# Kernel optimization log

Hardware: AMD Instinct MI355X
Metric: run time of the kernel (lower is better)

The kernel has to match this reference:

```python
import jax, jax.numpy as jnp
import numpy as np

B, H, S, D = 2, 16, 2048, 128
BS = 128  # block_size
NB = S // BS  # num_blocks
SPARSITY_PROB = 0.5


def setup_inputs() -> dict:
    key = jax.random.key(0)
    kq, kk, kv, km = jax.random.split(key, 4)
    query = jax.random.normal(kq, (B, H, S, D), dtype=jnp.float32)
    k_ = jax.random.normal(kk, (B, H, S, D), dtype=jnp.float32)
    v_ = jax.random.normal(kv, (B, H, S, D), dtype=jnp.float32)
    # block pattern: rand < sparsity_prob, diagonal forced True (causal=False)
    block_mask = jax.random.uniform(km, (NB, NB)) < SPARSITY_PROB
    block_mask = block_mask | jnp.eye(NB, dtype=bool)
    return {"query": query, "key": k_, "value": v_,
            "block_mask": block_mask, "block_size": BS}


def reference(query, key, value, block_mask, block_size):
    b, h, s, d = query.shape
    nb = s // block_size
    scale = 1.0 / jnp.sqrt(jnp.float32(d))
    # reshape into blocks: (b, h, nb, bs, d)
    qb = query.reshape(b, h, nb, block_size, d)
    kb = key.reshape(b, h, nb, block_size, d)
    vb = value.reshape(b, h, nb, block_size, d)
    # per-(i,j)-block scores: (b, h, i, j, q, k)
    scores = jnp.einsum('bhiqd,bhjkd->bhijqk', qb, kb) * scale
    # IMPORTANT: softmax is taken independently within each block (axis=-1),
    # matching the original's per-block (non-merged) softmax.
    attn = jax.nn.softmax(scores, axis=-1)
    # zero out inactive blocks, then sum contributions over j
    attn = attn * block_mask[None, None, :, :, None, None].astype(attn.dtype)
    out = jnp.einsum('bhijqk,bhjkd->bhiqd', attn, vb)
    return out.reshape(b, h, s, d)
```

## Files before the change

### kernel.cpp

```cpp
#include <hip/hip_runtime.h>
#include <stdint.h>

#define CBDIM 256
#define WBDIM 256
#define DBDIM 512

#if __has_builtin(__builtin_amdgcn_permlane32_swap) && \
    __has_builtin(__builtin_amdgcn_permlane16_swap)
#define HAVE_PERMLANE_SWAP 1
#else
#define HAVE_PERMLANE_SWAP 0
#endif

typedef __attribute__((ext_vector_type(8))) short short8;
typedef __attribute__((ext_vector_type(4))) float f32x4;

__device__ __forceinline__ unsigned f2bf(float f) {
    union { float f; unsigned u; } a; a.f = f;
    unsigned r = a.u + 0x7fffu + ((a.u >> 16) & 1u);
    return (r >> 16) & 0xffffu;
}
__device__ __forceinline__ unsigned cvtpk_bf16(float a, float b) {
    unsigned r;
    asm("v_cvt_pk_bf16_f32 %0, %1, %2" : "=v"(r) : "v"(a), "v"(b));
    return r;
}
__device__ __forceinline__ float f4e(float4 v, int e) {
    return e == 0 ? v.x : e == 1 ? v.y : e == 2 ? v.z : v.w;
}
__device__ __forceinline__ unsigned u4e(uint4 v, int e) {
    return e == 0 ? v.x : e == 1 ? v.y : e == 2 ? v.z : v.w;
}
__device__ __forceinline__ uint2 shfl_u2(uint2 v, int src) {
    uint2 r;
    r.x = (unsigned)__shfl((int)v.x, src);
    r.y = (unsigned)__shfl((int)v.y, src);
    return r;
}
__device__ __forceinline__ float xor16_f(float x, int lane) {
#if HAVE_PERMLANE_SWAP
    unsigned u = __float_as_uint(x);
    auto r = __builtin_amdgcn_permlane16_swap(u, u, false, false);
    return __uint_as_float((lane & 16) ? r[0] : r[1]);
#else
    return __shfl_xor(x, 16);
#endif
}
__device__ __forceinline__ float xor32_f(float x, int lane) {
#if HAVE_PERMLANE_SWAP
    unsigned u = __float_as_uint(x);
    auto r = __builtin_amdgcn_permlane32_swap(u, u, false, false);
    return __uint_as_float((lane & 32) ? r[0] : r[1]);
#else
    return __shfl_xor(x, 32);
#endif
}
__device__ __forceinline__ bool detect_bf16(const void* p) {
    unsigned w = ((const unsigned*)p)[threadIdx.x & 63];
    unsigned lo = w & 0xffffu, ex = (lo >> 7) & 0xffu;
    bool pl = (lo == 0u) || (ex >= 0x68u && ex <= 0x86u);
    return __popcll(__ballot(pl)) >= 40;
}
__device__ __forceinline__ void gload_lds16(const void* g, void* l) {
    __builtin_amdgcn_global_load_lds(
        (const __attribute__((address_space(1))) void*)g,
        (__attribute__((address_space(3))) void*)l, 16, 0, 0);
}

__global__ __launch_bounds__(CBDIM)
void convert_fused(const void* __restrict__ Ksrc, const void* __restrict__ Vsrc,
                   uint4* __restrict__ Kw, uint4* __restrict__ Vt,
                   const unsigned char* __restrict__ Mb, int* __restrict__ order,
                   int nIdsK)
{
    const int tid = threadIdx.x;
    const int b = blockIdx.x;
    if (b < 512) {
        bool isBf = detect_bf16(Vsrc);
        if (b == 0 && tid < 64) {
            int tt = tid;
            unsigned mu = ((const unsigned*)Mb)[tt];
            bool maskByte = (__ballot((mu & 0xFFFFFF00u) != 0u) != 0ull);
            int cnt = 0;
            if (tt < 16)
                for (int j = 0; j < 16; ++j) {
                    bool a = maskByte ? (Mb[tt * 16 + j] != 0)
                                      : (((const int*)Mb)[tt * 16 + j] != 0);
                    cnt += a ? 1 : 0;
                }
            int rank = 0;
            for (int j = 0; j < 16; ++j) {
                int cj = __shfl(cnt, j);
                if (cj > cnt || (cj == cnt && j < tt)) ++rank;
            }
            if (tt < 16) order[rank] = tt;
        }
        const size_t kb = (size_t)b * 16384;
        char* base = (char*)(Vt + (size_t)b * 2048);
#pragma unroll
        for (int it = 0; it < 2; ++it) {
            int id = it * CBDIM + tid, pp = id & 31, dc = id >> 5;
            if (isBf) {
                const unsigned short* vb = (const unsigned short*)Vsrc + kb
                                           + (size_t)(4 * pp) * 128 + dc * 8;
                uint4 r0 = *(const uint4*)(vb);
                uint4 r1 = *(const uint4*)(vb + 128);
                uint4 r2 = *(const uint4*)(vb + 256);
                uint4 r3 = *(const uint4*)(vb + 384);
#pragma unroll
                for (int e = 0; e < 8; ++e) {
                    unsigned h0 = u4e(r0, e >> 1), h1 = u4e(r1, e >> 1);
                    unsigned h2 = u4e(r2, e >> 1), h3 = u4e(r3, e >> 1);
                    if (e & 1) { h0 >>= 16; h1 >>= 16; h2 >>= 16; h3 >>= 16; }
                    uint2 pk;
                    pk.x = (h0 & 0xffffu) | (h1 << 16);
                    pk.y = (h2 & 0xffffu) | (h3 << 16);
                    int d = dc * 8 + e;
                    *(uint2*)(base + d * 256 + (((pp >> 1) ^ (d & 7)) << 4)
                              + ((pp & 1) << 3)) = pk;
                }
            } else {
                const float* vb = (const float*)Vsrc + kb
                                  + (size_t)(4 * pp) * 128 + dc * 8;
                float4 ra[4], rb[4];
#pragma unroll
                for (int r = 0; r < 4; ++r) {
                    ra[r] = *(const float4*)(vb + (size_t)r * 128);
                    rb[r] = *(const float4*)(vb + (size_t)r * 128 + 4);
                }
#pragma unroll
                for (int e = 0; e < 8; ++e) {
                    float v0 = (e < 4) ? f4e(ra[0], e) : f4e(rb[0], e - 4);
                    float v1 = (e < 4) ? f4e(ra[1], e) : f4e(rb[1], e - 4);
                    float v2 = (e < 4) ? f4e(ra[2], e) : f4e(rb[2], e - 4);
                    float v3 = (e < 4) ? f4e(ra[3], e) : f4e(rb[3], e - 4);
                    uint2 pk;
                    pk.x = f2bf(v0) | (f2bf(v1) << 16);
                    pk.y = f2bf(v2) | (f2bf(v3) << 16);
                    int d = dc * 8 + e;
                    *(uint2*)(base + d * 256 + (((pp >> 1) ^ (d & 7)) << 4)
                              + ((pp & 1) << 3)) = pk;
                }
            }
        }
    } else {
        bool isBf = detect_bf16(Ksrc);
        int stride = ((int)gridDim.x - 512) * CBDIM;
        for (int id = (b - 512) * CBDIM + tid; id < nIdsK; id += stride) {
            int lid = id & 2047, tt = id >> 11;
            int r = lid >> 4, c = (lid & 15) ^ (r & 7);
            size_t eo = (size_t)tt * 16384 + (size_t)r * 128 + c * 8;
            uint4 w;
            if (isBf) {
                w = *(const uint4*)((const unsigned short*)Ksrc + eo);
            } else {
                const float* p = (const float*)Ksrc + eo;
                float4 f0 = *(const float4*)p, f1 = *(const float4*)(p + 4);
                w.x = f2bf(f0.x) | (f2bf(f0.y) << 16);
                w.y = f2bf(f0.z) | (f2bf(f0.w) << 16);
                w.z = f2bf(f1.x) | (f2bf(f1.y) << 16);
                w.w = f2bf(f1.z) | (f2bf(f1.w) << 16);
            }
            Kw[id] = w;
        }
    }
}

template<bool QF32>
__device__ __forceinline__ void attn_core(const void* Qv, const uint4* Kw,
                                          const uint4* Vt, unsigned actm,
                                          void* Ov, char* ldsK, char* ldsV,
                                          int bh, int i)
{
    constexpr int S = 2048, D = 128;
    const int tid  = threadIdx.x;
    const int lane = tid & 63;
    const int wv   = tid >> 6;
    const int quad = lane >> 4;
    const int l16  = lane & 15;

    const int qb0 = wv * 32;
    const size_t qrowbase = ((size_t)bh * S + (size_t)i * 128) * D;

    short8 qf[2][4];
#pragma unroll
    for (int nt = 0; nt < 2; ++nt) {
        int qrow = qb0 + nt * 16 + l16;
#pragma unroll
        for (int ks = 0; ks < 4; ++ks) {
            int dof = ks * 32 + quad * 8;
            if constexpr (QF32) {
                const float* qp = (const float*)Qv + qrowbase + (size_t)qrow * D + dof;
                float4 f0 = *(const float4*)qp;
                float4 f1 = *(const float4*)(qp + 4);
                short8 v;
                v[0] = (short)f2bf(f0.x); v[1] = (short)f2bf(f0.y);
                v[2] = (short)f2bf(f0.z); v[3] = (short)f2bf(f0.w);
                v[4] = (short)f2bf(f1.x); v[5] = (short)f2bf(f1.y);
                v[6] = (short)f2bf(f1.z); v[7] = (short)f2bf(f1.w);
                qf[nt][ks] = v;
            } else {
                qf[nt][ks] = *(const short8*)((const unsigned short*)Qv
                              + qrowbase + (size_t)qrow * D + dof);
            }
        }
    }

    f32x4 accO[2][8];
#pragma unroll
    for (int a = 0; a < 2; ++a)
#pragma unroll
        for (int b = 0; b < 8; ++b)
            accO[a][b] = (f32x4){0.f, 0.f, 0.f, 0.f};

    const float C2 = 0.08838834764831845f * 1.44269504088896f;

    auto STAGE = [&](const uint4* t, char* lds) {
#pragma unroll
        for (int it = 0; it < 8; ++it) {
            int id = it * WBDIM + tid;
            int lo = (it * WBDIM + wv * 64) * 16;
            gload_lds16(t + id, lds + lo);
        }
        asm volatile("" ::: "memory");
    };
    auto ktile = [&](int jj) { return Kw + (size_t)(bh * 16 + jj) * 2048; };
    auto vtile = [&](int jj) { return Vt + (size_t)(bh * 16 + jj) * 2048; };

    int j = (int)__builtin_ctz(actm);
    unsigned m = actm & (actm - 1);

    STAGE(ktile(j), ldsK);
    STAGE(vtile(j), ldsV);
    asm volatile("s_waitcnt vmcnt(8)" ::: "memory");
    asm volatile("s_barrier" ::: "memory");

    while (true) {
        int jn = m ? (int)__builtin_ctz(m) : -1;
        if (jn >= 0) m &= m - 1;

        f32x4 accS[2][8];
#pragma unroll
        for (int nt = 0; nt < 2; ++nt)
#pragma unroll
            for (int mt = 0; mt < 8; ++mt)
                accS[nt][mt] = (f32x4){0.f, 0.f, 0.f, 0.f};

#pragma unroll
        for (int mt = 0; mt < 8; ++mt) {
            int r = mt * 16 + l16;
            short8 kf[4];
#pragma unroll
            for (int ks = 0; ks < 4; ++ks) {
                int c = ks * 4 + quad;
                kf[ks] = *(const short8*)(ldsK + r * 256 + ((c ^ (r & 7)) << 4));
            }
            __builtin_amdgcn_s_setprio(1);
#pragma unroll
            for (int nt = 0; nt < 2; ++nt)
#pragma unroll
                for (int ks = 0; ks < 4; ++ks)
                    accS[nt][mt] = __builtin_amdgcn_mfma_f32_16x16x32_bf16(
                        kf[ks], qf[nt][ks], accS[nt][mt], 0, 0, 0);
            __builtin_amdgcn_s_setprio(0);
        }

        uint2 p2[2][8];
#pragma unroll
        for (int nt = 0; nt < 2; ++nt) {
            float ps[8];
#pragma unroll
            for (int mt = 0; mt < 8; ++mt) {
                f32x4 p;
#pragma unroll
                for (int rr = 0; rr < 4; ++rr)
                    p[rr] = exp2f(accS[nt][mt][rr] * C2);
                accS[nt][mt] = p;
                ps[mt] = (p[0] + p[1]) + (p[2] + p[3]);
            }
            float sum = ((ps[0] + ps[1]) + (ps[2] + ps[3]))
                      + ((ps[4] + ps[5]) + (ps[6] + ps[7]));
            sum += xor16_f(sum, lane);
            sum += xor32_f(sum, lane);
            float rinv = __builtin_amdgcn_rcpf(sum);
#pragma unroll
            for (int mt = 0; mt < 8; ++mt) {
                p2[nt][mt].x = cvtpk_bf16(accS[nt][mt][0] * rinv,
                                          accS[nt][mt][1] * rinv);
                p2[nt][mt].y = cvtpk_bf16(accS[nt][mt][2] * rinv,
                                          accS[nt][mt][3] * rinv);
            }
        }

        asm volatile("s_waitcnt vmcnt(0)" ::: "memory");
        asm volatile("s_barrier" ::: "memory");
        if (jn >= 0) STAGE(ktile(jn), ldsK);

#pragma unroll
        for (int ks = 0; ks < 4; ++ks) {
            short8 pf[2];
#pragma unroll
            for (int nt = 0; nt < 2; ++nt) {
#if HAVE_PERMLANE_SWAP
                unsigned ax = p2[nt][2 * ks + 0].x, ay = p2[nt][2 * ks + 0].y;
                unsigned bx = p2[nt][2 * ks + 1].x, by = p2[nt][2 * ks + 1].y;
                auto rx = __builtin_amdgcn_permlane32_swap(ax, bx, false, false);
                auto ry = __builtin_amdgcn_permlane32_swap(ay, by, false, false);
                auto sx = __builtin_amdgcn_permlane16_swap(rx[0], rx[1], false, false);
                auto sy = __builtin_amdgcn_permlane16_swap(ry[0], ry[1], false, false);
                union { uint4 u; short8 s; } w;
                w.u.x = sx[0]; w.u.y = sy[0]; w.u.z = sx[1]; w.u.w = sy[1];
                pf[nt] = w.s;
#else
                const int srcA = l16 + ((quad & 1) << 5);
                const int srcB = srcA + 16;
                const bool hiMs = (quad >> 1) != 0;
                uint2 a0 = shfl_u2(p2[nt][2 * ks + 0], srcA);
                uint2 a1 = shfl_u2(p2[nt][2 * ks + 1], srcA);
                uint2 b0 = shfl_u2(p2[nt][2 * ks + 0], srcB);
                uint2 b1 = shfl_u2(p2[nt][2 * ks + 1], srcB);
                uint2 lo, hi;
                lo.x = hiMs ? a1.x : a0.x;  lo.y = hiMs ? a1.y : a0.y;
                hi.x = hiMs ? b1.x : b0.x;  hi.y = hiMs ? b1.y : b0.y;
                union { uint4 u; short8 s; } w;
                w.u.x = lo.x; w.u.y = lo.y; w.u.z = hi.x; w.u.w = hi.y;
                pf[nt] = w.s;
#endif
            }
            __builtin_amdgcn_s_setprio(1);
#pragma unroll
            for (int dt = 0; dt < 8; ++dt) {
                int d = dt * 16 + l16;
                int c = ks * 4 + quad;
                short8 vf = *(const short8*)(ldsV + d * 256 + ((c ^ (d & 7)) << 4));
                accO[0][dt] = __builtin_amdgcn_mfma_f32_16x16x32_bf16(
                    pf[0], vf, accO[0][dt], 0, 0, 0);
                accO[1][dt] = __builtin_amdgcn_mfma_f32_16x16x32_bf16(
                    pf[1], vf, accO[1][dt], 0, 0, 0);
            }
            __builtin_amdgcn_s_setprio(0);
        }

        if (jn < 0) break;
        asm volatile("s_waitcnt vmcnt(0)" ::: "memory");
        asm volatile("s_barrier" ::: "memory");
        STAGE(vtile(jn), ldsV);
        j = jn;
    }

#pragma unroll
    for (int mt = 0; mt < 2; ++mt)
#pragma unroll
        for (int rr = 0; rr < 4; ++rr) {
            int qrow = qb0 + mt * 16 + quad * 4 + rr;
#pragma unroll
            for (int nt = 0; nt < 8; ++nt) {
                size_t idx = qrowbase + (size_t)qrow * D + nt * 16 + l16;
                if constexpr (QF32)
                    ((float*)Ov)[idx] = accO[mt][nt][rr];
                else
                    ((unsigned short*)Ov)[idx] = (unsigned short)f2bf(accO[mt][nt][rr]);
            }
        }
}

__global__ __launch_bounds__(WBDIM, 2)
void attn_ws(const void* __restrict__ Q, const uint4* __restrict__ Kw,
             const uint4* __restrict__ Vt, const unsigned char* __restrict__ Mb,
             const int* __restrict__ order, void* __restrict__ O)
{
    __shared__ uint4 ldsK4[2048];
    __shared__ uint4 ldsV4[2048];
    int blk = blockIdx.x;
    int bh = ((blk >> 7) << 3) | (blk & 7);
    int slot = (blk >> 3) & 15;
    int i = order[(blk >> 8) ? (15 - slot) : slot];
    bool qBf = detect_bf16(Q);
    unsigned mu = ((const unsigned*)Mb)[threadIdx.x & 63];
    bool maskByte = (__ballot((mu & 0xFFFFFF00u) != 0u) != 0ull);
    unsigned actm = 0;
#pragma unroll
    for (int j = 0; j < 16; ++j) {
        bool a = maskByte ? (Mb[i * 16 + j] != 0)
                          : (((const int*)Mb)[i * 16 + j] != 0);
        actm |= (a ? 1u : 0u) << j;
    }
    if (qBf)
        attn_core<false>(Q, Kw, Vt, actm, O, (char*)ldsK4, (char*)ldsV4, bh, i);
    else
        attn_core<true>(Q, Kw, Vt, actm, O, (char*)ldsK4, (char*)ldsV4, bh, i);
}

template<bool QF32, bool KVF32>
__device__ __forceinline__ void attn_body(const void* Qv, const void* Kv,
                                          const void* Vv,
                                          const unsigned char* Mb, bool maskByte,
                                          void* Ov, char* ldsK, char* ldsV,
                                          int bh, int i)
{
    constexpr int S = 2048, D = 128;
    const int tid  = threadIdx.x;
    const int lane = tid & 63;
    const int wave = tid >> 6;
    const int quad = lane >> 4;
    const int l16  = lane & 15;

    const int qb0 = wave * 16;
    const size_t qrowbase = ((size_t)bh * S + (size_t)i * 128) * D;

    short8 qf[4];
    {
        int qrow = qb0 + l16;
#pragma unroll
        for (int ks = 0; ks < 4; ++ks) {
            int dof = ks * 32 + quad * 8;
            if constexpr (QF32) {
                const float* qp = (const float*)Qv + qrowbase + (size_t)qrow * D + dof;
                float4 f0 = *(const float4*)qp;
                float4 f1 = *(const float4*)(qp + 4);
                short8 v;
                v[0] = (short)f2bf(f0.x); v[1] = (short)f2bf(f0.y);
                v[2] = (short)f2bf(f0.z); v[3] = (short)f2bf(f0.w);
                v[4] = (short)f2bf(f1.x); v[5] = (short)f2bf(f1.y);
                v[6] = (short)f2bf(f1.z); v[7] = (short)f2bf(f1.w);
                qf[ks] = v;
            } else {
                qf[ks] = *(const short8*)((const unsigned short*)Qv
                          + qrowbase + (size_t)qrow * D + dof);
            }
        }
    }

    f32x4 accO[8];
#pragma unroll
    for (int b = 0; b < 8; ++b)
        accO[b] = (f32x4){0.f, 0.f, 0.f, 0.f};

    const float C2 = 0.08838834764831845f * 1.44269504088896f;
    const int srcA = l16 + ((quad & 1) << 5);
    const int srcB = srcA + 16;
    const bool hiMs = (quad >> 1) != 0;

    for (int j = 0; j < 16; ++j) {
        bool active = maskByte ? (Mb[i * 16 + j] != 0)
                               : (((const int*)Mb)[i * 16 + j] != 0);
        if (!active) continue;

        __syncthreads();
        const size_t kb = ((size_t)bh * S + (size_t)j * 128) * D;

        if constexpr (KVF32) {
#pragma unroll
            for (int it = 0; it < 8; ++it) {
                int f = it * DBDIM + tid;
                int r = f >> 5, c4 = f & 31;
                float4 v = ((const float4*)((const float*)Kv + kb))[f];
                uint2 pk;
                pk.x = f2bf(v.x) | (f2bf(v.y) << 16);
                pk.y = f2bf(v.z) | (f2bf(v.w) << 16);
                int ch = c4 >> 1;
                *(uint2*)(ldsK + r * 256 + ((ch ^ (r & 7)) << 4)
                          + ((c4 & 1) << 3)) = pk;
            }
        } else {
#pragma unroll
            for (int it = 0; it < 4; ++it) {
                int id = it * DBDIM + tid;
                int r = id >> 4, ch = id & 15;
                uint4 v = ((const uint4*)((const unsigned short*)Kv + kb))[id];
                *(uint4*)(ldsK + r * 256 + ((ch ^ (r & 7)) << 4)) = v;
            }
        }

        {
            int id = tid, pp = id & 31, dc = id >> 5;
            if constexpr (KVF32) {
                const float* vb = (const float*)Vv + kb + (size_t)(4 * pp) * D + dc * 8;
                float4 ra[4], rb[4];
#pragma unroll
                for (int r = 0; r < 4; ++r) {
                    ra[r] = *(const float4*)(vb + (size_t)r * D);
                    rb[r] = *(const float4*)(vb + (size_t)r * D + 4);
                }
#pragma unroll
                for (int e = 0; e < 8; ++e) {
                    float v0 = (e < 4) ? f4e(ra[0], e) : f4e(rb[0], e - 4);
                    float v1 = (e < 4) ? f4e(ra[1], e) : f4e(rb[1], e - 4);
                    float v2 = (e < 4) ? f4e(ra[2], e) : f4e(rb[2], e - 4);
                    float v3 = (e < 4) ? f4e(ra[3], e) : f4e(rb[3], e - 4);
                    uint2 pk;
                    pk.x = f2bf(v0) | (f2bf(v1) << 16);
                    pk.y = f2bf(v2) | (f2bf(v3) << 16);
                    int d = dc * 8 + e;
                    *(uint2*)(ldsV + d * 256 + (((pp >> 1) ^ (d & 7)) << 4)
                              + ((pp & 1) << 3)) = pk;
                }
            } else {
                const unsigned short* vb = (const unsigned short*)Vv + kb
                                           + (size_t)(4 * pp) * D + dc * 8;
                uint4 r0 = *(const uint4*)(vb);
                uint4 r1 = *(const uint4*)(vb + D);
                uint4 r2 = *(const uint4*)(vb + 2 * D);
                uint4 r3 = *(const uint4*)(vb + 3 * D);
#pragma unroll
                for (int e = 0; e < 8; ++e) {
                    unsigned h0 = u4e(r0, e >> 1), h1 = u4e(r1, e >> 1);
                    unsigned h2 = u4e(r2, e >> 1), h3 = u4e(r3, e >> 1);
                    if (e & 1) { h0 >>= 16; h1 >>= 16; h2 >>= 16; h3 >>= 16; }
                    uint2 pk;
                    pk.x = (h0 & 0xffffu) | (h1 << 16);
                    pk.y = (h2 & 0xffffu) | (h3 << 16);
                    int d = dc * 8 + e;
                    *(uint2*)(ldsV + d * 256 + (((pp >> 1) ^ (d & 7)) << 4)
                              + ((pp & 1) << 3)) = pk;
                }
            }
        }
        __syncthreads();

        f32x4 accS[8];
#pragma unroll
        for (int mt = 0; mt < 8; ++mt)
            accS[mt] = (f32x4){0.f, 0.f, 0.f, 0.f};

#pragma unroll
        for (int mt = 0; mt < 8; ++mt) {
            int r = mt * 16 + l16;
            short8 kf[4];
#pragma unroll
            for (int ks = 0; ks < 4; ++ks) {
                int c = ks * 4 + quad;
                kf[ks] = *(const short8*)(ldsK + r * 256 + ((c ^ (r & 7)) << 4));
            }
#pragma unroll
            for (int ks = 0; ks < 4; ++ks)
                accS[mt] = __builtin_amdgcn_mfma_f32_16x16x32_bf16(
                    kf[ks], qf[ks], accS[mt], 0, 0, 0);
        }

        float ps[8];
#pragma unroll
        for (int mt = 0; mt < 8; ++mt) {
            f32x4 p;
#pragma unroll
            for (int rr = 0; rr < 4; ++rr)
                p[rr] = exp2f(accS[mt][rr] * C2);
            accS[mt] = p;
            ps[mt] = (p[0] + p[1]) + (p[2] + p[3]);
        }
        float sum = ((ps[0] + ps[1]) + (ps[2] + ps[3]))
                  + ((ps[4] + ps[5]) + (ps[6] + ps[7]));
        sum += __shfl_xor(sum, 16);
        sum += __shfl_xor(sum, 32);
        float rinv = 1.0f / sum;

        uint2 p2[8];
#pragma unroll
        for (int mt = 0; mt < 8; ++mt) {
            p2[mt].x = f2bf(accS[mt][0] * rinv) | (f2bf(accS[mt][1] * rinv) << 16);
            p2[mt].y = f2bf(accS[mt][2] * rinv) | (f2bf(accS[mt][3] * rinv) << 16);
        }

#pragma unroll
        for (int ks = 0; ks < 4; ++ks) {
            short8 pf;
            {
                uint2 a0 = shfl_u2(p2[2 * ks + 0], srcA);
                uint2 a1 = shfl_u2(p2[2 * ks + 1], srcA);
                uint2 b0 = shfl_u2(p2[2 * ks + 0], srcB);
                uint2 b1 = shfl_u2(p2[2 * ks + 1], srcB);
                uint2 lo, hi;
                lo.x = hiMs ? a1.x : a0.x;  lo.y = hiMs ? a1.y : a0.y;
                hi.x = hiMs ? b1.x : b0.x;  hi.y = hiMs ? b1.y : b0.y;
                union { uint4 u; short8 s; } w;
                w.u.x = lo.x; w.u.y = lo.y; w.u.z = hi.x; w.u.w = hi.y;
                pf = w.s;
            }
#pragma unroll
            for (int dt = 0; dt < 8; ++dt) {
                int d = dt * 16 + l16;
                int c = ks * 4 + quad;
                short8 vf = *(const short8*)(ldsV + d * 256 + ((c ^ (d & 7)) << 4));
                accO[dt] = __builtin_amdgcn_mfma_f32_16x16x32_bf16(
                    pf, vf, accO[dt], 0, 0, 0);
            }
        }
    }

#pragma unroll
    for (int rr = 0; rr < 4; ++rr) {
        int qrow = qb0 + quad * 4 + rr;
#pragma unroll
        for (int dt = 0; dt < 8; ++dt) {
            size_t idx = qrowbase + (size_t)qrow * D + dt * 16 + l16;
            if constexpr (QF32)
                ((float*)Ov)[idx] = accO[dt][rr];
            else
                ((unsigned short*)Ov)[idx] = (unsigned short)f2bf(accO[dt][rr]);
        }
    }
}

__global__ __launch_bounds__(DBDIM, 4)
void attn_direct(const void* __restrict__ Q, const void* __restrict__ K,
                 const void* __restrict__ V,
                 const unsigned char* __restrict__ Mb, void* __restrict__ O)
{
    __shared__ uint4 ldsK4[2048];
    __shared__ uint4 ldsV4[2048];
    int blk = blockIdx.x;
    int bh = ((blk >> 7) << 3) | (blk & 7);
    int i  = (blk >> 3) & 15;
    bool qBf = detect_bf16(Q);
    unsigned mu = ((const unsigned*)Mb)[threadIdx.x & 63];
    bool maskByte = (__ballot((mu & 0xFFFFFF00u) != 0u) != 0ull);
    if (qBf)
        attn_body<false, false>(Q, K, V, Mb, maskByte, O,
                                (char*)ldsK4, (char*)ldsV4, bh, i);
    else
        attn_body<true, true>(Q, K, V, Mb, maskByte, O,
                              (char*)ldsK4, (char*)ldsV4, bh, i);
}

extern "C" void kernel_launch(void* const* d_in, const int* in_sizes, int n_in,
                              void* d_out, int out_size, void* d_ws, size_t ws_size,
                              hipStream_t stream) {
    const int NIDS = 512 * 2048;
    const size_t need = (size_t)NIDS * 16 * 2 + 256;
    if (ws_size >= need) {
        uint4* Kw = (uint4*)d_ws;
        uint4* Vt = Kw + NIDS;
        int* order = (int*)(Vt + NIDS);
        convert_fused<<<1536, CBDIM, 0, stream>>>(d_in[1], d_in[2], Kw, Vt,
                                                  (const unsigned char*)d_in[3],
                                                  order, NIDS);
        attn_ws<<<512, WBDIM, 0, stream>>>(d_in[0], Kw, Vt,
                                           (const unsigned char*)d_in[3],
                                           order, d_out);
    } else {
        attn_direct<<<512, DBDIM, 0, stream>>>(d_in[0], d_in[1], d_in[2],
                                               (const unsigned char*)d_in[3], d_out);
    }
}
```

Baseline: 197.5 us.

## Split key dimension across two wave groups with LDS softmax-sum exchange

Doubles the attention block to 512 threads and splits each 128-key block between two groups of four waves. Each group computes half the scores and partial softmax sums, exchanges the row sums through a small shared buffer, and at the end reduces the two partial output accumulators through LDS. The aim is more waves in flight to hide MFMA and load latency, and lower per-wave register pressure. The cost is extra barriers and an LDS reduction pass. It also replaces exp2f with a raw v_exp_f32 instruction.

```diff
diff --git a/kernel.cpp b/kernel.cpp
--- a/kernel.cpp
+++ b/kernel.cpp
@@ -2,7 +2,7 @@
 #include <stdint.h>
 
 #define CBDIM 256
-#define WBDIM 256
+#define ABDIM 512
 #define DBDIM 512
 
 #if __has_builtin(__builtin_amdgcn_permlane32_swap) && \
@@ -23,6 +23,11 @@
 __device__ __forceinline__ unsigned cvtpk_bf16(float a, float b) {
     unsigned r;
     asm("v_cvt_pk_bf16_f32 %0, %1, %2" : "=v"(r) : "v"(a), "v"(b));
+    return r;
+}
+__device__ __forceinline__ float exp2_raw(float x) {
+    float r;
+    asm("v_exp_f32 %0, %1" : "=v"(r) : "v"(x));
     return r;
 }
 __device__ __forceinline__ float f4e(float4 v, int e) {
@@ -170,16 +175,18 @@
 __device__ __forceinline__ void attn_core(const void* Qv, const uint4* Kw,
                                           const uint4* Vt, unsigned actm,
                                           void* Ov, char* ldsK, char* ldsV,
-                                          int bh, int i)
+                                          float* ldsS, int bh, int i)
 {
     constexpr int S = 2048, D = 128;
     const int tid  = threadIdx.x;
     const int lane = tid & 63;
     const int wv   = tid >> 6;
+    const int wk   = wv >> 2;
+    const int wq   = wv & 3;
     const int quad = lane >> 4;
     const int l16  = lane & 15;
 
-    const int qb0 = wv * 32;
+    const int qb0 = wq * 32;
     const size_t qrowbase = ((size_t)bh * S + (size_t)i * 128) * D;
 
     short8 qf[2][4];
@@ -217,9 +224,9 @@
 
     auto STAGE = [&](const uint4* t, char* lds) {
 #pragma unroll
-        for (int it = 0; it < 8; ++it) {
-            int id = it * WBDIM + tid;
-            int lo = (it * WBDIM + wv * 64) * 16;
+        for (int it = 0; it < 4; ++it) {
+            int id = it * ABDIM + tid;
+            int lo = (it * ABDIM + wv * 64) * 16;
             gload_lds16(t + id, lds + lo);
         }
         asm volatile("" ::: "memory");
@@ -232,23 +239,23 @@
 
     STAGE(ktile(j), ldsK);
     STAGE(vtile(j), ldsV);
-    asm volatile("s_waitcnt vmcnt(8)" ::: "memory");
+    asm volatile("s_waitcnt vmcnt(4)" ::: "memory");
     asm volatile("s_barrier" ::: "memory");
 
     while (true) {
         int jn = m ? (int)__builtin_ctz(m) : -1;
         if (jn >= 0) m &= m - 1;
 
-        f32x4 accS[2][8];
+        f32x4 accS[2][4];
 #pragma unroll
         for (int nt = 0; nt < 2; ++nt)
 #pragma unroll
-            for (int mt = 0; mt < 8; ++mt)
+            for (int mt = 0; mt < 4; ++mt)
                 accS[nt][mt] = (f32x4){0.f, 0.f, 0.f, 0.f};
 
 #pragma unroll
-        for (int mt = 0; mt < 8; ++mt) {
-            int r = mt * 16 + l16;
+        for (int mt = 0; mt < 4; ++mt) {
+            int r = (wk << 6) + mt * 16 + l16;
             short8 kf[4];
 #pragma unroll
             for (int ks = 0; ks < 4; ++ks) {
@@ -265,26 +272,39 @@
             __builtin_amdgcn_s_setprio(0);
         }
 
-        uint2 p2[2][8];
+        float myh[2];
 #pragma unroll
         for (int nt = 0; nt < 2; ++nt) {
-            float ps[8];
-#pragma unroll
-            for (int mt = 0; mt < 8; ++mt) {
+            float ps[4];
+#pragma unroll
+            for (int mt = 0; mt < 4; ++mt) {
                 f32x4 p;
 #pragma unroll
                 for (int rr = 0; rr < 4; ++rr)
-                    p[rr] = exp2f(accS[nt][mt][rr] * C2);
+                    p[rr] = exp2_raw(accS[nt][mt][rr] * C2);
                 accS[nt][mt] = p;
                 ps[mt] = (p[0] + p[1]) + (p[2] + p[3]);
             }
-            float sum = ((ps[0] + ps[1]) + (ps[2] + ps[3]))
-                      + ((ps[4] + ps[5]) + (ps[6] + ps[7]));
+            float sum = (ps[0] + ps[1]) + (ps[2] + ps[3]);
             sum += xor16_f(sum, lane);
             sum += xor32_f(sum, lane);
-            float rinv = __builtin_amdgcn_rcpf(sum);
-#pragma unroll
-            for (int mt = 0; mt < 8; ++mt) {
+            myh[nt] = sum;
+            if (quad == 0)
+                ldsS[((wq * 2 + nt) * 2 + wk) * 16 + l16] = sum;
+        }
+
+        asm volatile("s_waitcnt vmcnt(0)" ::: "memory");
+        asm volatile("s_barrier" ::: "memory");
+        if (jn >= 0) STAGE(ktile(jn), ldsK);
+
+        uint2 p2[2][4];
+#pragma unroll
+        for (int nt = 0; nt < 2; ++nt) {
+            float full = myh[nt]
+                       + ldsS[((wq * 2 + nt) * 2 + (wk ^ 1)) * 16 + l16];
+            float rinv = __builtin_amdgcn_rcpf(full);
+#pragma unroll
+            for (int mt = 0; mt < 4; ++mt) {
                 p2[nt][mt].x = cvtpk_bf16(accS[nt][mt][0] * rinv,
                                           accS[nt][mt][1] * rinv);
                 p2[nt][mt].y = cvtpk_bf16(accS[nt][mt][2] * rinv,
@@ -292,18 +312,14 @@
             }
         }
 
-        asm volatile("s_waitcnt vmcnt(0)" ::: "memory");
-        asm volatile("s_barrier" ::: "memory");
-        if (jn >= 0) STAGE(ktile(jn), ldsK);
-
-#pragma unroll
-        for (int ks = 0; ks < 4; ++ks) {
+#pragma unroll
+        for (int ksl = 0; ksl < 2; ++ksl) {
             short8 pf[2];
 #pragma unroll
             for (int nt = 0; nt < 2; ++nt) {
 #if HAVE_PERMLANE_SWAP
-                unsigned ax = p2[nt][2 * ks + 0].x, ay = p2[nt][2 * ks + 0].y;
-                unsigned bx = p2[nt][2 * ks + 1].x, by = p2[nt][2 * ks + 1].y;
+                unsigned ax = p2[nt][2 * ksl + 0].x, ay = p2[nt][2 * ksl + 0].y;
+                unsigned bx = p2[nt][2 * ksl + 1].x, by = p2[nt][2 * ksl + 1].y;
                 auto rx = __builtin_amdgcn_permlane32_swap(ax, bx, false, false);
                 auto ry = __builtin_amdgcn_permlane32_swap(ay, by, false, false);
                 auto sx = __builtin_amdgcn_permlane16_swap(rx[0], rx[1], false, false);
@@ -315,10 +331,10 @@
                 const int srcA = l16 + ((quad & 1) << 5);
                 const int srcB = srcA + 16;
                 const bool hiMs = (quad >> 1) != 0;
-                uint2 a0 = shfl_u2(p2[nt][2 * ks + 0], srcA);
-                uint2 a1 = shfl_u2(p2[nt][2 * ks + 1], srcA);
-                uint2 b0 = shfl_u2(p2[nt][2 * ks + 0], srcB);
-                uint2 b1 = shfl_u2(p2[nt][2 * ks + 1], srcB);
+                uint2 a0 = shfl_u2(p2[nt][2 * ksl + 0], srcA);
+                uint2 a1 = shfl_u2(p2[nt][2 * ksl + 1], srcA);
+                uint2 b0 = shfl_u2(p2[nt][2 * ksl + 0], srcB);
+                uint2 b1 = shfl_u2(p2[nt][2 * ksl + 1], srcB);
                 uint2 lo, hi;
                 lo.x = hiMs ? a1.x : a0.x;  lo.y = hiMs ? a1.y : a0.y;
                 hi.x = hiMs ? b1.x : b0.x;  hi.y = hiMs ? b1.y : b0.y;
@@ -327,11 +343,11 @@
                 pf[nt] = w.s;
 #endif
             }
+            int c = (wk * 2 + ksl) * 4 + quad;
             __builtin_amdgcn_s_setprio(1);
 #pragma unroll
             for (int dt = 0; dt < 8; ++dt) {
                 int d = dt * 16 + l16;
-                int c = ks * 4 + quad;
                 short8 vf = *(const short8*)(ldsV + d * 256 + ((c ^ (d & 7)) << 4));
                 accO[0][dt] = __builtin_amdgcn_mfma_f32_16x16x32_bf16(
                     pf[0], vf, accO[0][dt], 0, 0, 0);
@@ -348,29 +364,58 @@
         j = jn;
     }
 
-#pragma unroll
-    for (int mt = 0; mt < 2; ++mt)
-#pragma unroll
-        for (int rr = 0; rr < 4; ++rr) {
-            int qrow = qb0 + mt * 16 + quad * 4 + rr;
-#pragma unroll
-            for (int nt = 0; nt < 8; ++nt) {
-                size_t idx = qrowbase + (size_t)qrow * D + nt * 16 + l16;
-                if constexpr (QF32)
-                    ((float*)Ov)[idx] = accO[mt][nt][rr];
-                else
-                    ((unsigned short*)Ov)[idx] = (unsigned short)f2bf(accO[mt][nt][rr]);
-            }
-        }
-}
-
-__global__ __launch_bounds__(WBDIM, 2)
+    asm volatile("s_waitcnt vmcnt(0)" ::: "memory");
+    asm volatile("s_barrier" ::: "memory");
+    char* exch = (wq < 2 ? ldsK : ldsV) + ((wq & 1) << 14);
+    if (wk == 1) {
+#pragma unroll
+        for (int nt = 0; nt < 2; ++nt)
+#pragma unroll
+            for (int dt = 0; dt < 8; ++dt) {
+                int idx = nt * 8 + dt;
+                *(f32x4*)(exch + lane * 256 + ((idx ^ (lane & 15)) << 4)) =
+                    accO[nt][dt];
+            }
+    }
+    asm volatile("s_barrier" ::: "memory");
+    if (wk == 0) {
+#pragma unroll
+        for (int nt = 0; nt < 2; ++nt)
+#pragma unroll
+            for (int dt = 0; dt < 8; ++dt) {
+                int idx = nt * 8 + dt;
+                f32x4 o = *(const f32x4*)(exch + lane * 256
+                                          + ((idx ^ (lane & 15)) << 4));
+#pragma unroll
+                for (int rr = 0; rr < 4; ++rr)
+                    accO[nt][dt][rr] += o[rr];
+            }
+#pragma unroll
+        for (int nt = 0; nt < 2; ++nt)
+#pragma unroll
+            for (int rr = 0; rr < 4; ++rr) {
+                int qrow = qb0 + nt * 16 + quad * 4 + rr;
+#pragma unroll
+                for (int dt = 0; dt < 8; ++dt) {
+                    size_t idx = qrowbase + (size_t)qrow * D + dt * 16 + l16;
+                    if constexpr (QF32)
+                        ((float*)Ov)[idx] = accO[nt][dt][rr];
+                    else
+                        ((unsigned short*)Ov)[idx] =
+                            (unsigned short)f2bf(accO[nt][dt][rr]);
+                }
+            }
+    }
+}
+
+__global__ __launch_bounds__(ABDIM, 4)
 void attn_ws(const void* __restrict__ Q, const uint4* __restrict__ Kw,
              const uint4* __restrict__ Vt, const unsigned char* __restrict__ Mb,
              const int* __restrict__ order, void* __restrict__ O)
 {
     __shared__ uint4 ldsK4[2048];
     __shared__ uint4 ldsV4[2048];
+    __shared__ float ldsS[256];
     int blk = blockIdx.x;
     int bh = ((blk >> 7) << 3) | (blk & 7);
     int slot = (blk >> 3) & 15;
@@ -386,9 +431,11 @@
         actm |= (a ? 1u : 0u) << j;
     }
     if (qBf)
-        attn_core<false>(Q, Kw, Vt, actm, O, (char*)ldsK4, (char*)ldsV4, bh, i);
+        attn_core<false>(Q, Kw, Vt, actm, O, (char*)ldsK4, (char*)ldsV4,
+                         ldsS, bh, i);
     else
-        attn_core<true>(Q, Kw, Vt, actm, O, (char*)ldsK4, (char*)ldsV4, bh, i);
+        attn_core<true>(Q, Kw, Vt, actm, O, (char*)ldsK4, (char*)ldsV4,
+                        ldsS, bh, i);
 }
 
 template<bool QF32, bool KVF32>
@@ -634,7 +681,7 @@
         convert_fused<<<1536, CBDIM, 0, stream>>>(d_in[1], d_in[2], Kw, Vt,
                                                   (const unsigned char*)d_in[3],
                                                   order, NIDS);
-        attn_ws<<<512, WBDIM, 0, stream>>>(d_in[0], Kw, Vt,
+        attn_ws<<<512, ABDIM, 0, stream>>>(d_in[0], Kw, Vt,
                                            (const unsigned char*)d_in[3],
                                            order, d_out);
     } else {
```

Measured after the change: 320.3 us. 1.62x slower.
